# Performance work log

Hardware: AMD Instinct MI355X
Metric: run time of the kernel (lower is better)

## Reference

```python
import jax, jax.numpy as jnp
import numpy as np

D_MODEL = 4096
D_BASE = 8192
K_SUB = 1024
N_TOK = 8192


def setup_inputs() -> dict:
    key = jax.random.key(0)
    k1, k2, k3, k4 = jax.random.split(key, 4)
    x = jax.random.normal(k1, (N_TOK, D_MODEL), dtype=jnp.float32)
    subspace_indices = jax.random.randint(k2, (K_SUB,), 0, D_BASE)
    # learned shared basis (orthogonal init approximated by scaled gaussian)
    U_base = jax.random.normal(k3, (D_MODEL, D_BASE), dtype=jnp.float32) / np.sqrt(D_MODEL)
    V_base = jax.random.normal(k4, (D_BASE, D_MODEL), dtype=jnp.float32) / np.sqrt(D_BASE)
    return {"x": x, "subspace_indices": subspace_indices, "U_base": U_base, "V_base": V_base}


def reference(x, subspace_indices, U_base, V_base):
    # gather active subspace columns/rows of the shared basis
    u_subset = U_base[:, subspace_indices]          # [d_model, k]
    v_subset = V_base[subspace_indices, :]          # [k, d_model]
    projected = jax.nn.silu(x @ u_subset)           # [n_tok, k]
    return projected @ v_subset                     # [n_tok, d_model]
```

## Files before the change

kernel.cpp:

```cpp
#include <hip/hip_runtime.h>
#include <hip/hip_bf16.h>
#include <stdint.h>

#define D_MODEL 4096
#define D_BASE  8192
#define K_SUB   1024
#define N_TOK   8192

typedef __attribute__((ext_vector_type(8))) short bf16x8;
typedef __attribute__((ext_vector_type(4))) float f32x4;

__device__ __forceinline__ unsigned short f2bf(float f) {
    union { float f; uint32_t u; } c; c.f = f;
    uint32_t u = c.u;
    uint32_t r = u + 0x7FFFu + ((u >> 16) & 1u);
    return (unsigned short)(r >> 16);
}

__device__ __forceinline__ void gload_lds16(const void* g, void* l) {
    __builtin_amdgcn_global_load_lds(
        (__attribute__((address_space(1))) void*)g,
        (__attribute__((address_space(3))) void*)l, 16, 0, 0);
}

#define VMCNT(N) do { __builtin_amdgcn_sched_barrier(0); \
    asm volatile("s_waitcnt vmcnt(" #N ")" ::: "memory"); } while (0)
#define PHASE_MID() do { __builtin_amdgcn_sched_barrier(0); __builtin_amdgcn_s_barrier(); \
    asm volatile("s_waitcnt lgkmcnt(0)" ::: "memory"); __builtin_amdgcn_sched_barrier(0); } while (0)
#define PHASE_END() do { __builtin_amdgcn_sched_barrier(0); __builtin_amdgcn_s_barrier(); } while (0)

__global__ void convert_x_kernel(const float* __restrict__ x, unsigned short* __restrict__ xb) {
    int t = blockIdx.x * 256 + threadIdx.x;
    const float4* p = (const float4*)x + (size_t)t * 2;
    float4 a = p[0], b = p[1];
    ushort4 lo, hi;
    lo.x = f2bf(a.x); lo.y = f2bf(a.y); lo.z = f2bf(a.z); lo.w = f2bf(a.w);
    hi.x = f2bf(b.x); hi.y = f2bf(b.y); hi.z = f2bf(b.z); hi.w = f2bf(b.w);
    *(ushort4*)(xb + (size_t)t * 8) = lo;
    *(ushort4*)(xb + (size_t)t * 8 + 4) = hi;
}

__global__ __launch_bounds__(256) void gather_u_t(const float* __restrict__ U,
                                                  const int* __restrict__ idx,
                                                  unsigned short* __restrict__ Ut) {
    __shared__ unsigned short tile[64][66];
    __shared__ int lidx[64];
    const int t = threadIdx.x;
    const int n0 = (blockIdx.x & 15) * 64;
    const int k0 = (blockIdx.x >> 4) * 64;
    if (t < 64) lidx[t] = idx[n0 + t];
    __syncthreads();
    const int c = t & 63, r4 = t >> 6;
    #pragma unroll
    for (int p = 0; p < 16; ++p) {
        int kr = p * 4 + r4;
        tile[c][kr] = f2bf(U[(size_t)(k0 + kr) * D_BASE + lidx[c]]);
    }
    __syncthreads();
    #pragma unroll
    for (int p = 0; p < 16; ++p) {
        int nr = p * 4 + r4;
        Ut[(size_t)(n0 + nr) * D_MODEL + k0 + c] = tile[nr][c];
    }
}

__global__ __launch_bounds__(256) void gather_v_t(const float* __restrict__ V,
                                                  const int* __restrict__ idx,
                                                  unsigned short* __restrict__ Vt) {
    __shared__ unsigned short tile[64][66];
    __shared__ int lidx[64];
    const int t = threadIdx.x;
    const int n0 = (blockIdx.x & 15) * 64;
    const int d0 = (blockIdx.x >> 4) * 64;
    if (t < 64) lidx[t] = idx[n0 + t];
    __syncthreads();
    const int c = t & 63, r4 = t >> 6;
    #pragma unroll
    for (int p = 0; p < 16; ++p) {
        int nr = p * 4 + r4;
        tile[nr][c] = f2bf(V[(size_t)lidx[nr] * D_MODEL + d0 + c]);
    }
    __syncthreads();
    #pragma unroll
    for (int p = 0; p < 16; ++p) {
        int dr = p * 4 + r4;
        Vt[(size_t)(d0 + dr) * K_SUB + n0 + c] = tile[c][dr];
    }
}

template<int MH>
__device__ __forceinline__ void mma_h(f32x4 (&acc)[8][2],
                                      const bf16x8 (&af)[4][2], const bf16x8 (&bfr)[2][2]) {
    __builtin_amdgcn_s_setprio(1);
    #pragma unroll
    for (int m = 0; m < 4; ++m)
        #pragma unroll
        for (int n = 0; n < 2; ++n)
            #pragma unroll
            for (int ks = 0; ks < 2; ++ks)
                acc[MH * 4 + m][n] = __builtin_amdgcn_mfma_f32_16x16x32_bf16(
                    af[m][ks], bfr[n][ks], acc[MH * 4 + m][n], 0, 0, 0);
    __builtin_amdgcn_s_setprio(0);
}

__global__ __launch_bounds__(512, 2)
void gemm1_8p(const unsigned short* __restrict__ A, const unsigned short* __restrict__ Bt,
              unsigned short* __restrict__ C) {
    constexpr int K = D_MODEL, N = K_SUB, NT = K / 64;
    __shared__ __align__(16) unsigned short lds[49152];

    const int t = threadIdx.x, lane = t & 63, w = t >> 6;
    const int wr = w >> 2, wc = w & 3;
    const int lr = lane & 15, lk = lane >> 4;

    const int f = blockIdx.x;
    const int g = (f & 7) * 32 + (f >> 3);
    const int m0 = (g >> 3) * 256, n0 = (g & 7) * 128;

    const int cswz0 = ((lk ^ (lr & 7)) * 8);
    const int cswz1 = (((4 + lk) ^ (lr & 7)) * 8);
    const int srow = lane >> 3;
    const int scol = ((lane & 7) ^ srow) * 8;

    auto stage_A = [&](int kt, int mh) {
        const unsigned short* src = A + (size_t)(m0 + mh * 128) * K + kt * 64;
        unsigned short* dst = &lds[(kt & 1) * 24576 + mh * 8192];
        #pragma unroll
        for (int i = 0; i < 2; ++i) {
            int c = i * 8 + w;
            gload_lds16(src + (size_t)(c * 8 + srow) * K + scol, dst + c * 512);
        }
    };
    auto stage_B = [&](int kt) {
        const unsigned short* src = Bt + (size_t)n0 * K + kt * 64;
        unsigned short* dst = &lds[(kt & 1) * 24576 + 16384];
        #pragma unroll
        for (int i = 0; i < 2; ++i) {
            int c = i * 8 + w;
            gload_lds16(src + (size_t)(c * 8 + srow) * K + scol, dst + c * 512);
        }
    };
    auto read_A = [&](int kt, int mh, bf16x8 (&af)[4][2]) {
        const unsigned short* base = &lds[(kt & 1) * 24576 + mh * 8192];
        #pragma unroll
        for (int m = 0; m < 4; ++m) {
            int rw = wr * 64 + m * 16 + lr;
            af[m][0] = *(const bf16x8*)(base + rw * 64 + cswz0);
            af[m][1] = *(const bf16x8*)(base + rw * 64 + cswz1);
        }
    };
    auto read_B = [&](int kt, bf16x8 (&bfr)[2][2]) {
        const unsigned short* base = &lds[(kt & 1) * 24576 + 16384];
        #pragma unroll
        for (int n = 0; n < 2; ++n) {
            int rw = wc * 32 + n * 16 + lr;
            bfr[n][0] = *(const bf16x8*)(base + rw * 64 + cswz0);
            bfr[n][1] = *(const bf16x8*)(base + rw * 64 + cswz1);
        }
    };

    f32x4 acc[8][2] = {};

    stage_B(0); stage_A(0, 0); stage_A(0, 1); stage_B(1); stage_A(1, 0);
    VMCNT(6);
    __builtin_amdgcn_s_barrier();
    __builtin_amdgcn_sched_barrier(0);

    for (int kt = 0; kt < NT; kt += 2) {
        const bool more = (kt + 2 < NT);
        bf16x8 bf0[2][2], bf1[2][2];
        {
            bf16x8 af[4][2];
            read_A(kt, 0, af); read_B(kt, bf0);
            stage_A(kt + 1, 1);
            PHASE_MID();
            mma_h<0>(acc, af, bf0);
            VMCNT(6);
            PHASE_END();
        }
        {
            bf16x8 af[4][2];
            read_A(kt, 1, af);
            if (more) stage_B(kt + 2);
            PHASE_MID();
            mma_h<1>(acc, af, bf0);
            if (more) { VMCNT(4); } else { VMCNT(2); }
            PHASE_END();
        }
        {
            bf16x8 af[4][2];
            read_A(kt + 1, 0, af); read_B(kt + 1, bf1);
            if (more) { stage_A(kt + 2, 0); stage_A(kt + 2, 1); }
            PHASE_MID();
            mma_h<0>(acc, af, bf1);
            if (more) { VMCNT(6); } else { VMCNT(0); }
            PHASE_END();
        }
        {
            bf16x8 af[4][2];
            read_A(kt + 1, 1, af);
            if (kt + 3 < NT) { stage_B(kt + 3); stage_A(kt + 3, 0); }
            PHASE_MID();
            mma_h<1>(acc, af, bf1);
            if (more) VMCNT(6);
            PHASE_END();
        }
    }

    #pragma unroll
    for (int mh = 0; mh < 2; ++mh)
        #pragma unroll
        for (int m = 0; m < 4; ++m)
            #pragma unroll
            for (int n = 0; n < 2; ++n)
                #pragma unroll
                for (int r = 0; r < 4; ++r) {
                    int row = m0 + mh * 128 + wr * 64 + m * 16 + lk * 4 + r;
                    int col = n0 + wc * 32 + n * 16 + lr;
                    float v = acc[mh * 4 + m][n][r];
                    v = v / (1.0f + __expf(-v));
                    C[(size_t)row * N + col] = f2bf(v);
                }
}

__global__ __launch_bounds__(512, 2)
void gemm2_8p(const unsigned short* __restrict__ A, const unsigned short* __restrict__ Bt,
              float* __restrict__ C) {
    constexpr int K = K_SUB, N = D_MODEL, NT = K / 64;
    constexpr int BUFSZ = 32768;
    __shared__ __align__(16) unsigned short lds[2 * BUFSZ];

    const int t = threadIdx.x, lane = t & 63, w = t >> 6;
    const int wr = w >> 2, wc = w & 3;
    const int lr = lane & 15, lk = lane >> 4;

    const int f = blockIdx.x;
    const int g = (f & 7) * 64 + (f >> 3);
    const int m0 = (g >> 4) * 256, n0 = (g & 15) * 256;

    const int cswz0 = ((lk ^ (lr & 7)) * 8);
    const int cswz1 = (((4 + lk) ^ (lr & 7)) * 8);
    const int srow = lane >> 3;
    const int scol = ((lane & 7) ^ srow) * 8;

    auto stage_A = [&](int kt, int mh) {
        const unsigned short* src = A + (size_t)(m0 + mh * 128) * K + kt * 64;
        unsigned short* dst = &lds[(kt & 1) * BUFSZ + mh * 8192];
        #pragma unroll
        for (int i = 0; i < 2; ++i) {
            int c = i * 8 + w;
            gload_lds16(src + (size_t)(c * 8 + srow) * K + scol, dst + c * 512);
        }
    };
    auto stage_B = [&](int kt, int nh) {
        const unsigned short* src = Bt + (size_t)(n0 + nh * 128) * K + kt * 64;
        unsigned short* dst = &lds[(kt & 1) * BUFSZ + 16384 + nh * 8192];
        #pragma unroll
        for (int i = 0; i < 2; ++i) {
            int c = i * 8 + w;
            gload_lds16(src + (size_t)(c * 8 + srow) * K + scol, dst + c * 512);
        }
    };
    auto read_A = [&](int kt, int mh, bf16x8 (&af)[4][2]) {
        const unsigned short* base = &lds[(kt & 1) * BUFSZ + mh * 8192];
        #pragma unroll
        for (int m = 0; m < 4; ++m) {
            int rw = wr * 64 + m * 16 + lr;
            af[m][0] = *(const bf16x8*)(base + rw * 64 + cswz0);
            af[m][1] = *(const bf16x8*)(base + rw * 64 + cswz1);
        }
    };
    auto read_B = [&](int kt, int nh, bf16x8 (&bfr)[2][2]) {
        const unsigned short* base = &lds[(kt & 1) * BUFSZ + 16384 + nh * 8192];
        #pragma unroll
        for (int n = 0; n < 2; ++n) {
            int rw = wc * 32 + n * 16 + lr;
            bfr[n][0] = *(const bf16x8*)(base + rw * 64 + cswz0);
            bfr[n][1] = *(const bf16x8*)(base + rw * 64 + cswz1);
        }
    };

    f32x4 acc[8][4] = {};

    stage_A(0, 0); stage_B(0, 0); stage_B(0, 1); stage_A(0, 1);
    stage_A(1, 0); stage_B(1, 1); stage_A(1, 1);
    VMCNT(6);
    __builtin_amdgcn_s_barrier();
    __builtin_amdgcn_sched_barrier(0);

    for (int kt = 0; kt < NT; ++kt) {
        bf16x8 af[4][2], bf0[2][2], bf1[2][2];
        {
            read_A(kt, 0, af); read_B(kt, 0, bf0);
            if (kt + 1 < NT) stage_B(kt + 1, 0);
            PHASE_MID();
            __builtin_amdgcn_s_setprio(1);
            #pragma unroll
            for (int m = 0; m < 4; ++m)
                #pragma unroll
                for (int n = 0; n < 2; ++n)
                    #pragma unroll
                    for (int ks = 0; ks < 2; ++ks)
                        acc[m][n] = __builtin_amdgcn_mfma_f32_16x16x32_bf16(
                            af[m][ks], bf0[n][ks], acc[m][n], 0, 0, 0);
            __builtin_amdgcn_s_setprio(0);
            PHASE_END();
        }
        {
            read_B(kt, 1, bf1);
            if (kt + 2 < NT) stage_A(kt + 2, 0);
            PHASE_MID();
            __builtin_amdgcn_s_setprio(1);
            #pragma unroll
            for (int m = 0; m < 4; ++m)
                #pragma unroll
                for (int n = 0; n < 2; ++n)
                    #pragma unroll
                    for (int ks = 0; ks < 2; ++ks)
                        acc[m][2 + n] = __builtin_amdgcn_mfma_f32_16x16x32_bf16(
                            af[m][ks], bf1[n][ks], acc[m][2 + n], 0, 0, 0);
            __builtin_amdgcn_s_setprio(0);
            PHASE_END();
        }
        {
            read_A(kt, 1, af);
            if (kt + 2 < NT) stage_B(kt + 2, 1);
            PHASE_MID();
            __builtin_amdgcn_s_setprio(1);
            #pragma unroll
            for (int m = 0; m < 4; ++m)
                #pragma unroll
                for (int n = 0; n < 2; ++n)
                    #pragma unroll
                    for (int ks = 0; ks < 2; ++ks)
                        acc[4 + m][n] = __builtin_amdgcn_mfma_f32_16x16x32_bf16(
                            af[m][ks], bf0[n][ks], acc[4 + m][n], 0, 0, 0);
            __builtin_amdgcn_s_setprio(0);
            PHASE_END();
        }
        {
            if (kt + 2 < NT) stage_A(kt + 2, 1);
            PHASE_MID();
            __builtin_amdgcn_s_setprio(1);
            #pragma unroll
            for (int m = 0; m < 4; ++m)
                #pragma unroll
                for (int n = 0; n < 2; ++n)
                    #pragma unroll
                    for (int ks = 0; ks < 2; ++ks)
                        acc[4 + m][2 + n] = __builtin_amdgcn_mfma_f32_16x16x32_bf16(
                            af[m][ks], bf1[n][ks], acc[4 + m][2 + n], 0, 0, 0);
            __builtin_amdgcn_s_setprio(0);
            __builtin_amdgcn_sched_barrier(0);
            if (kt < NT - 2) { VMCNT(6); }
            else if (kt == NT - 2) { VMCNT(0); }
            PHASE_END();
        }
    }

    #pragma unroll
    for (int mh = 0; mh < 2; ++mh)
        #pragma unroll
        for (int nh = 0; nh < 2; ++nh)
            #pragma unroll
            for (int m = 0; m < 4; ++m)
                #pragma unroll
                for (int n = 0; n < 2; ++n)
                    #pragma unroll
                    for (int r = 0; r < 4; ++r) {
                        int row = m0 + mh * 128 + wr * 64 + m * 16 + lk * 4 + r;
                        int col = n0 + nh * 128 + wc * 32 + n * 16 + lr;
                        C[(size_t)row * N + col] = acc[mh * 4 + m][nh * 2 + n][r];
                    }
}

extern "C" void kernel_launch(void* const* d_in, const int* in_sizes, int n_in,
                              void* d_out, int out_size, void* d_ws, size_t ws_size,
                              hipStream_t stream) {
    const float* x   = (const float*)d_in[0];
    const int*   idx = (const int*)d_in[1];
    const float* U   = (const float*)d_in[2];
    const float* V   = (const float*)d_in[3];
    float* out = (float*)d_out;

    unsigned short* Ut = (unsigned short*)d_ws;
    unsigned short* Vt = Ut + (size_t)K_SUB * D_MODEL;
    unsigned short* P  = Vt + (size_t)K_SUB * D_MODEL;
    unsigned short* xb = (unsigned short*)d_out;

    convert_x_kernel<<<(N_TOK * D_MODEL) / (256 * 8), 256, 0, stream>>>(x, xb);
    gather_u_t<<<(K_SUB / 64) * (D_MODEL / 64), 256, 0, stream>>>(U, idx, Ut);
    gather_v_t<<<(K_SUB / 64) * (D_MODEL / 64), 256, 0, stream>>>(V, idx, Vt);

    gemm1_8p<<<256, 512, 0, stream>>>(xb, Ut, P);
    gemm2_8p<<<512, 512, 0, stream>>>(P, Vt, out);
}
```

Measured before the change: 244.5 us.

## Rework gemm1 warp tiling to 4x2 layout and restructure U gather

The first GEMM's 8 waves change from a 2x4 grid (each wave 128x32 split into two M halves) to a 4x2 grid (each wave 64x64). Each wave now holds 4x4 accumulators and reads B in two halves, which changes the ratio of LDS fragment reads to MFMA work. The pipeline is reorganised to stage A and B tiles one k-step ahead. Separately, the U gather kernel now handles a 32-row strip across all 1024 selected columns per block, reusing the loaded indices and writing vectorised ushort4 rows, at the cost of far fewer blocks and a large LDS tile.

```diff
diff --git a/kernel.cpp b/kernel.cpp
--- a/kernel.cpp
+++ b/kernel.cpp
@@ -40,27 +40,34 @@
     *(ushort4*)(xb + (size_t)t * 8 + 4) = hi;
 }
 
-__global__ __launch_bounds__(256) void gather_u_t(const float* __restrict__ U,
+__global__ __launch_bounds__(256) void gather_u_s(const float* __restrict__ U,
                                                   const int* __restrict__ idx,
                                                   unsigned short* __restrict__ Ut) {
-    __shared__ unsigned short tile[64][66];
-    __shared__ int lidx[64];
+    __shared__ unsigned short tile[1024 * 36];
+    __shared__ int lidx[1024];
     const int t = threadIdx.x;
-    const int n0 = (blockIdx.x & 15) * 64;
-    const int k0 = (blockIdx.x >> 4) * 64;
-    if (t < 64) lidx[t] = idx[n0 + t];
+    const int k0 = blockIdx.x * 32;
+    #pragma unroll
+    for (int i = 0; i < 4; ++i) lidx[i * 256 + t] = idx[i * 256 + t];
     __syncthreads();
-    const int c = t & 63, r4 = t >> 6;
-    #pragma unroll
-    for (int p = 0; p < 16; ++p) {
-        int kr = p * 4 + r4;
-        tile[c][kr] = f2bf(U[(size_t)(k0 + kr) * D_BASE + lidx[c]]);
+    for (int kr = 0; kr < 32; ++kr) {
+        const float* Urow = U + (size_t)(k0 + kr) * D_BASE;
+        #pragma unroll
+        for (int it = 0; it < 4; ++it) {
+            int n = it * 256 + t;
+            tile[n * 36 + kr] = f2bf(Urow[lidx[n]]);
+        }
     }
     __syncthreads();
     #pragma unroll
-    for (int p = 0; p < 16; ++p) {
-        int nr = p * 4 + r4;
-        Ut[(size_t)(n0 + nr) * D_MODEL + k0 + c] = tile[nr][c];
+    for (int r = 0; r < 4; ++r) {
+        int n = r * 256 + t;
+        unsigned short* drow = Ut + (size_t)n * D_MODEL + k0;
+        #pragma unroll
+        for (int j = 0; j < 8; ++j) {
+            ushort4 v = *(const ushort4*)&tile[n * 36 + j * 4];
+            *(ushort4*)(drow + j * 4) = v;
+        }
     }
 }
 
@@ -88,21 +95,6 @@
     }
 }
 
-template<int MH>
-__device__ __forceinline__ void mma_h(f32x4 (&acc)[8][2],
-                                      const bf16x8 (&af)[4][2], const bf16x8 (&bfr)[2][2]) {
-    __builtin_amdgcn_s_setprio(1);
-    #pragma unroll
-    for (int m = 0; m < 4; ++m)
-        #pragma unroll
-        for (int n = 0; n < 2; ++n)
-            #pragma unroll
-            for (int ks = 0; ks < 2; ++ks)
-                acc[MH * 4 + m][n] = __builtin_amdgcn_mfma_f32_16x16x32_bf16(
-                    af[m][ks], bfr[n][ks], acc[MH * 4 + m][n], 0, 0, 0);
-    __builtin_amdgcn_s_setprio(0);
-}
-
 __global__ __launch_bounds__(512, 2)
 void gemm1_8p(const unsigned short* __restrict__ A, const unsigned short* __restrict__ Bt,
               unsigned short* __restrict__ C) {
@@ -110,7 +102,7 @@
     __shared__ __align__(16) unsigned short lds[49152];
 
     const int t = threadIdx.x, lane = t & 63, w = t >> 6;
-    const int wr = w >> 2, wc = w & 3;
+    const int wm = w >> 1, wn = w & 1;
     const int lr = lane & 15, lk = lane >> 4;
 
     const int f = blockIdx.x;
@@ -122,13 +114,13 @@
     const int srow = lane >> 3;
     const int scol = ((lane & 7) ^ srow) * 8;
 
-    auto stage_A = [&](int kt, int mh) {
-        const unsigned short* src = A + (size_t)(m0 + mh * 128) * K + kt * 64;
-        unsigned short* dst = &lds[(kt & 1) * 24576 + mh * 8192];
+    auto stage_A = [&](int kt, int half) {
+        const unsigned short* src = A + (size_t)(m0 + half * 128) * K + kt * 64;
+        unsigned short* dst = &lds[(kt & 1) * 24576 + half * 8192];
         #pragma unroll
         for (int i = 0; i < 2; ++i) {
-            int c = i * 8 + w;
-            gload_lds16(src + (size_t)(c * 8 + srow) * K + scol, dst + c * 512);
+            int c2 = i * 8 + w;
+            gload_lds16(src + (size_t)(c2 * 8 + srow) * K + scol, dst + c2 * 512);
         }
     };
     auto stage_B = [&](int kt) {
@@ -136,91 +128,118 @@
         unsigned short* dst = &lds[(kt & 1) * 24576 + 16384];
         #pragma unroll
         for (int i = 0; i < 2; ++i) {
-            int c = i * 8 + w;
-            gload_lds16(src + (size_t)(c * 8 + srow) * K + scol, dst + c * 512);
-        }
-    };
-    auto read_A = [&](int kt, int mh, bf16x8 (&af)[4][2]) {
-        const unsigned short* base = &lds[(kt & 1) * 24576 + mh * 8192];
+            int c2 = i * 8 + w;
+            gload_lds16(src + (size_t)(c2 * 8 + srow) * K + scol, dst + c2 * 512);
+        }
+    };
+    auto read_A = [&](int kt, bf16x8 (&af)[4][2]) {
+        const unsigned short* base = &lds[(kt & 1) * 24576 + (wm >> 1) * 8192];
         #pragma unroll
         for (int m = 0; m < 4; ++m) {
-            int rw = wr * 64 + m * 16 + lr;
+            int rw = (wm & 1) * 64 + m * 16 + lr;
             af[m][0] = *(const bf16x8*)(base + rw * 64 + cswz0);
             af[m][1] = *(const bf16x8*)(base + rw * 64 + cswz1);
         }
     };
-    auto read_B = [&](int kt, bf16x8 (&bfr)[2][2]) {
+    auto read_B2 = [&](int kt, int nh, bf16x8 (&bfr)[2][2]) {
         const unsigned short* base = &lds[(kt & 1) * 24576 + 16384];
         #pragma unroll
         for (int n = 0; n < 2; ++n) {
-            int rw = wc * 32 + n * 16 + lr;
+            int rw = wn * 64 + (nh * 2 + n) * 16 + lr;
             bfr[n][0] = *(const bf16x8*)(base + rw * 64 + cswz0);
             bfr[n][1] = *(const bf16x8*)(base + rw * 64 + cswz1);
         }
     };
 
-    f32x4 acc[8][2] = {};
-
-    stage_B(0); stage_A(0, 0); stage_A(0, 1); stage_B(1); stage_A(1, 0);
-    VMCNT(6);
+    f32x4 acc[4][4] = {};
+
+    stage_A(0, 0); stage_A(0, 1); stage_B(0); stage_A(1, 0);
+    VMCNT(2);
     __builtin_amdgcn_s_barrier();
     __builtin_amdgcn_sched_barrier(0);
 
     for (int kt = 0; kt < NT; kt += 2) {
         const bool more = (kt + 2 < NT);
-        bf16x8 bf0[2][2], bf1[2][2];
-        {
-            bf16x8 af[4][2];
-            read_A(kt, 0, af); read_B(kt, bf0);
-            stage_A(kt + 1, 1);
-            PHASE_MID();
-            mma_h<0>(acc, af, bf0);
-            VMCNT(6);
-            PHASE_END();
-        }
-        {
-            bf16x8 af[4][2];
-            read_A(kt, 1, af);
-            if (more) stage_B(kt + 2);
-            PHASE_MID();
-            mma_h<1>(acc, af, bf0);
-            if (more) { VMCNT(4); } else { VMCNT(2); }
-            PHASE_END();
-        }
-        {
-            bf16x8 af[4][2];
-            read_A(kt + 1, 0, af); read_B(kt + 1, bf1);
-            if (more) { stage_A(kt + 2, 0); stage_A(kt + 2, 1); }
-            PHASE_MID();
-            mma_h<0>(acc, af, bf1);
-            if (more) { VMCNT(6); } else { VMCNT(0); }
-            PHASE_END();
-        }
-        {
-            bf16x8 af[4][2];
-            read_A(kt + 1, 1, af);
-            if (kt + 3 < NT) { stage_B(kt + 3); stage_A(kt + 3, 0); }
-            PHASE_MID();
-            mma_h<1>(acc, af, bf1);
-            if (more) VMCNT(6);
-            PHASE_END();
-        }
-    }
-
-    #pragma unroll
-    for (int mh = 0; mh < 2; ++mh)
-        #pragma unroll
-        for (int m = 0; m < 4; ++m)
-            #pragma unroll
-            for (int n = 0; n < 2; ++n)
-                #pragma unroll
-                for (int r = 0; r < 4; ++r) {
-                    int row = m0 + mh * 128 + wr * 64 + m * 16 + lk * 4 + r;
-                    int col = n0 + wc * 32 + n * 16 + lr;
-                    float v = acc[mh * 4 + m][n][r];
-                    v = v / (1.0f + __expf(-v));
-                    C[(size_t)row * N + col] = f2bf(v);
-                }
+        {
+            bf16x8 af[4][2], bfr[2][2];
+            read_A(kt, af); read_B2(kt, 0, bfr);
+            stage_A(kt + 1, 1); stage_B(kt + 1);
+            PHASE_MID();
+            __builtin_amdgcn_s_setprio(1);
+            #pragma unroll
+            for (int m = 0; m < 4; ++m)
+                #pragma unroll
+                for (int n = 0; n < 2; ++n)
+                    #pragma unroll
+                    for (int ks = 0; ks < 2; ++ks)
+                        acc[m][n] = __builtin_amdgcn_mfma_f32_16x16x32_bf16(
+                            af[m][ks], bfr[n][ks], acc[m][n], 0, 0, 0);
+            __builtin_amdgcn_s_setprio(0);
+            PHASE_END();
+            bf16x8 bfr2[2][2];
+            read_B2(kt, 1, bfr2);
+            if (more) stage_A(kt + 2, 0);
+            PHASE_MID();
+            __builtin_amdgcn_s_setprio(1);
+            #pragma unroll
+            for (int m = 0; m < 4; ++m)
+                #pragma unroll
+                for (int n = 0; n < 2; ++n)
+                    #pragma unroll
+                    for (int ks = 0; ks < 2; ++ks)
+                        acc[m][2 + n] = __builtin_amdgcn_mfma_f32_16x16x32_bf16(
+                            af[m][ks], bfr2[n][ks], acc[m][2 + n], 0, 0, 0);
+            __builtin_amdgcn_s_setprio(0);
+            if (more) { VMCNT(2); } else { VMCNT(0); }
+            PHASE_END();
+        }
+        {
+            bf16x8 af[4][2], bfr[2][2];
+            read_A(kt + 1, af); read_B2(kt + 1, 0, bfr);
+            if (more) { stage_A(kt + 2, 1); stage_B(kt + 2); }
+            PHASE_MID();
+            __builtin_amdgcn_s_setprio(1);
+            #pragma unroll
+            for (int m = 0; m < 4; ++m)
+                #pragma unroll
+                for (int n = 0; n < 2; ++n)
+                    #pragma unroll
+                    for (int ks = 0; ks < 2; ++ks)
+                        acc[m][n] = __builtin_amdgcn_mfma_f32_16x16x32_bf16(
+                            af[m][ks], bfr[n][ks], acc[m][n], 0, 0, 0);
+            __builtin_amdgcn_s_setprio(0);
+            PHASE_END();
+            bf16x8 bfr2[2][2];
+            read_B2(kt + 1, 1, bfr2);
+            if (more) stage_A(kt + 3, 0);
+            PHASE_MID();
+            __builtin_amdgcn_s_setprio(1);
+            #pragma unroll
+            for (int m = 0; m < 4; ++m)
+                #pragma unroll
+                for (int n = 0; n < 2; ++n)
+                    #pragma unroll
+                    for (int ks = 0; ks < 2; ++ks)
+                        acc[m][2 + n] = __builtin_amdgcn_mfma_f32_16x16x32_bf16(
+                            af[m][ks], bfr2[n][ks], acc[m][2 + n], 0, 0, 0);
+            __builtin_amdgcn_s_setprio(0);
+            if (more) VMCNT(2);
+            PHASE_END();
+        }
+    }
+
+    #pragma unroll
+    for (int m = 0; m < 4; ++m)
+        #pragma unroll
+        for (int n = 0; n < 4; ++n)
+            #pragma unroll
+            for (int r = 0; r < 4; ++r) {
+                int row = m0 + wm * 64 + m * 16 + lk * 4 + r;
+                int col = n0 + wn * 64 + n * 16 + lr;
+                float v = acc[m][n][r];
+                v = v / (1.0f + __expf(-v));
+                C[(size_t)row * N + col] = f2bf(v);
+            }
 }
 
 __global__ __launch_bounds__(512, 2)
@@ -248,8 +267,8 @@
         unsigned short* dst = &lds[(kt & 1) * BUFSZ + mh * 8192];
         #pragma unroll
         for (int i = 0; i < 2; ++i) {
-            int c = i * 8 + w;
-            gload_lds16(src + (size_t)(c * 8 + srow) * K + scol, dst + c * 512);
+            int c2 = i * 8 + w;
+            gload_lds16(src + (size_t)(c2 * 8 + srow) * K + scol, dst + c2 * 512);
         }
     };
     auto stage_B = [&](int kt, int nh) {
@@ -257,8 +276,8 @@
         unsigned short* dst = &lds[(kt & 1) * BUFSZ + 16384 + nh * 8192];
         #pragma unroll
         for (int i = 0; i < 2; ++i) {
-            int c = i * 8 + w;
-            gload_lds16(src + (size_t)(c * 8 + srow) * K + scol, dst + c * 512);
+            int c2 = i * 8 + w;
+            gload_lds16(src + (size_t)(c2 * 8 + srow) * K + scol, dst + c2 * 512);
         }
     };
     auto read_A = [&](int kt, int mh, bf16x8 (&af)[4][2]) {
@@ -389,7 +408,7 @@
     unsigned short* xb = (unsigned short*)d_out;
 
     convert_x_kernel<<<(N_TOK * D_MODEL) / (256 * 8), 256, 0, stream>>>(x, xb);
-    gather_u_t<<<(K_SUB / 64) * (D_MODEL / 64), 256, 0, stream>>>(U, idx, Ut);
+    gather_u_s<<<D_MODEL / 32, 256, 0, stream>>>(U, idx, Ut);
     gather_v_t<<<(K_SUB / 64) * (D_MODEL / 64), 256, 0, stream>>>(V, idx, Vt);
 
     gemm1_8p<<<256, 512, 0, stream>>>(xb, Ut, P);
```

After: 241.8 us. No clear change (-1.1%).
